# Kernel optimization log

Measured on AMD Instinct MI355X. Metric: run time of the kernel, lower is better.

The kernel has to match this reference:

```python
import jax, jax.numpy as jnp
import numpy as np

T, N, E, F, G, H = 8, 100000, 1600000, 17, 32, 48


def setup_inputs() -> dict:
    key = jax.random.key(0)
    ks = jax.random.split(key, 24)
    p = lambda k, sh: jax.random.normal(k, sh, jnp.float32) * 0.05
    return {
        "node_features": jax.random.normal(ks[0], (T, N, F), jnp.float32),
        "edge_index": jax.random.randint(ks[1], (T, 2, E), 0, N, jnp.int32),
        "graph_features": jax.random.normal(ks[2], (T, G), jnp.float32),
        # conv1 / conv2 (self + neigh linears)
        "Ws1": p(ks[3], (H, F)), "bs1": jnp.zeros((H,), jnp.float32),
        "Wn1": p(ks[4], (H, F)), "bn1": jnp.zeros((H,), jnp.float32),
        "Ws2": p(ks[5], (H, H)), "bs2": jnp.zeros((H,), jnp.float32),
        "Wn2": p(ks[6], (H, H)), "bn2": jnp.zeros((H,), jnp.float32),
        # graph projection
        "Wgp": p(ks[7], (H, G)), "bgp": jnp.zeros((H,), jnp.float32),
        # GRU (input 2H, hidden H), torch layout [3H, in]
        "W_ih": p(ks[8], (3 * H, 2 * H)), "b_ih": jnp.zeros((3 * H,), jnp.float32),
        "W_hh": p(ks[9], (3 * H, H)), "b_hh": jnp.zeros((3 * H,), jnp.float32),
        # attention, spatial mask, temporal mask
        "Wa": p(ks[10], (1, H)), "ba": jnp.zeros((1,), jnp.float32),
        "Wsm": p(ks[11], (H, H)), "bsm": jnp.zeros((H,), jnp.float32),
        "Wtm": p(ks[12], (1, H)), "btm": jnp.zeros((1,), jnp.float32),
        "Wr1": p(ks[13], (H, H)), "br1": jnp.zeros((H,), jnp.float32),
        "Wr2": p(ks[14], (1, H)), "br2": jnp.zeros((1,), jnp.float32),
    }


def _conv(x, src, dst, Ws, bs, Wn, bn):
    # gather-scatter mean aggregation over edges, then dual linear + relu
    n = x.shape[0]
    agg = jax.ops.segment_sum(x[src], dst, num_segments=n)          # [N, d]
    deg = jax.ops.segment_sum(jnp.ones(dst.shape, x.dtype), dst, num_segments=n)
    neigh = agg / jnp.clip(deg, 1.0)[:, None]
    return jax.nn.relu(x @ Ws.T + bs + neigh @ Wn.T + bn)


def _forward(node_features, edge_index, graph_features,
             Ws1, bs1, Wn1, bn1, Ws2, bs2, Wn2, bn2, Wgp, bgp,
             W_ih, b_ih, W_hh, b_hh, Wa, ba, Wsm, bsm, Wtm, btm,
             Wr1, br1, Wr2, br2):
    def snap(_, inp):
        x, src, dst, gf = inp
        h = _conv(x, src, dst, Ws1, bs1, Wn1, bn1)
        h = _conv(h, src, dst, Ws2, bs2, Wn2, bn2)
        sm = jax.nn.sigmoid(h @ Wsm.T + bsm)                        # [N, H]
        h = h * sm
        pooled = h.mean(axis=0)                                     # [H]
        gs = jax.nn.relu(gf @ Wgp.T + bgp)                          # [H]
        return None, (jnp.concatenate([pooled, gs]), sm)

    _, (seq, spatial_masks) = jax.lax.scan(
        snap, None,
        (node_features, edge_index[:, 0], edge_index[:, 1], graph_features))
    # seq: [T, 2H]

    def gru_step(h, x):
        gi = x @ W_ih.T + b_ih
        gh = h @ W_hh.T + b_hh
        ir, iz, inn = jnp.split(gi, 3)
        hr, hz, hn = jnp.split(gh, 3)
        r = jax.nn.sigmoid(ir + hr)
        z = jax.nn.sigmoid(iz + hz)
        n = jnp.tanh(inn + r * hn)
        h_new = (1.0 - z) * n + z * h
        return h_new, h_new

    h0 = jnp.zeros((H,), seq.dtype)
    _, gru_out = jax.lax.scan(gru_step, h0, seq)                    # [T, H]

    temp_mask = jax.nn.sigmoid(gru_out @ Wtm.T + btm)[:, 0]         # [T]
    scores = (gru_out @ Wa.T + ba)[:, 0]                            # [T]
    weights = jax.nn.softmax(scores)
    context = jnp.sum(gru_out * (weights * temp_mask)[:, None], axis=0)  # [H]
    pred = (jax.nn.relu(context @ Wr1.T + br1) @ Wr2.T + br2)[0]    # scalar

    top8 = jax.lax.top_k(jnp.abs(Ws1).mean(axis=0), 8)[0]           # channel importance values
    return pred, weights, top8, spatial_masks, temp_mask


def reference(node_features, edge_index, graph_features,
              Ws1, bs1, Wn1, bn1, Ws2, bs2, Wn2, bn2, Wgp, bgp,
              W_ih, b_ih, W_hh, b_hh, Wa, ba, Wsm, bsm, Wtm, btm,
              Wr1, br1, Wr2, br2):
    return _forward(node_features, edge_index, graph_features,
                    Ws1, bs1, Wn1, bn1, Ws2, bs2, Wn2, bn2, Wgp, bgp,
                    W_ih, b_ih, W_hh, b_hh, Wa, ba, Wsm, bsm, Wtm, btm,
                    Wr1, br1, Wr2, br2)
```

## Files before the change

kernel.cpp:

```cpp
#include <hip/hip_runtime.h>
#include <math.h>

#define T_ 8
#define N_ 100000
#define E_ 1600000
#define F_ 17
#define G_ 32
#define H_ 48
#define CONV_GRID 2048
#define FP 20
#define BK_ 128
#define NBK 782
#define CAP 2560
#define HIST_BLK 98
#define NPW 8

__device__ __forceinline__ float bf2f(unsigned short u) {
    return __uint_as_float((unsigned)u << 16);
}
__device__ __forceinline__ unsigned short f2bf(float v) {
    unsigned u = __float_as_uint(v);
    u += 0x7FFFu + ((u >> 16) & 1u);
    return (unsigned short)(u >> 16);
}

__global__ void k_binit(int* __restrict__ bcur) {
    int i = blockIdx.x * 1024 + threadIdx.x;
    if (i < NBK) bcur[i] = i * CAP;
}

__global__ __launch_bounds__(1024) void k_bscat(const int* __restrict__ src,
                                                const int* __restrict__ dst,
                                                int* __restrict__ bcur,
                                                unsigned* __restrict__ pairs) {
    __shared__ int cur[NBK];
    __shared__ int hist[NBK];
    int tid = threadIdx.x;
    for (int i = tid; i < NBK; i += 1024) hist[i] = 0;
    __syncthreads();
    int base = blockIdx.x * 16384;
    unsigned p[16]; int bk[16];
#pragma unroll
    for (int k = 0; k < 16; ++k) {
        int e = base + k * 1024 + tid;
        if (e < E_) {
            int d = dst[e];
            p[k] = (unsigned)src[e] | ((unsigned)(d & 127) << 17);
            bk[k] = d >> 7;
            atomicAdd(&hist[bk[k]], 1);
        } else {
            bk[k] = -1;
        }
    }
    __syncthreads();
    for (int i = tid; i < NBK; i += 1024) {
        int h = hist[i];
        cur[i] = h ? atomicAdd(&bcur[i], h) : 0;
    }
    __syncthreads();
#pragma unroll
    for (int k = 0; k < 16; ++k) {
        if (bk[k] >= 0) {
            int pos = atomicAdd(&cur[bk[k]], 1);
            if (pos < (bk[k] + 1) * CAP - 8) pairs[pos] = p[k];
        }
    }
}

__global__ __launch_bounds__(256) void k_sort(
        const unsigned* __restrict__ pairs, int* __restrict__ bcur,
        int* __restrict__ srcs, int* __restrict__ rowp, int* __restrict__ rowe) {
    __shared__ int hist[BK_];
    __shared__ int scan[BK_];
    __shared__ int curs[BK_];
    __shared__ int cnt_s;
    int tid = threadIdx.x, b = blockIdx.x;
    int start = b * CAP;
    if (tid == 0) {
        int c = bcur[b] - start;
        cnt_s = (c < CAP - 8) ? c : (CAP - 8);
        bcur[b] = start;
    }
    if (tid < BK_) hist[tid] = 0;
    __syncthreads();
    int count = cnt_s;
    int stop = start + count;
    for (int e = start + tid; e < stop; e += 256)
        atomicAdd(&hist[pairs[e] >> 17], 1);
    __syncthreads();
    if (tid < BK_) scan[tid] = hist[tid];
    __syncthreads();
    for (int off = 1; off < BK_; off <<= 1) {
        int v = 0;
        if (tid < BK_ && tid >= off) v = scan[tid - off];
        __syncthreads();
        if (tid < BK_) scan[tid] += v;
        __syncthreads();
    }
    if (tid < BK_) {
        int n = b * BK_ + tid;
        if (n < N_) {
            int st = start + scan[tid] - hist[tid];
            rowp[n] = st;
            rowe[n] = st + hist[tid];
            curs[tid] = st;
        }
    }
    __syncthreads();
    for (int e = start + tid; e < stop; e += 256) {
        unsigned p = pairs[e];
        int loc = (int)(p >> 17);
        int pos = atomicAdd(&curs[loc], 1);
        srcs[pos] = (int)(p & 131071u);
    }
    if (tid < 8) srcs[stop + tid] = 0;
}

__global__ __launch_bounds__(256) void k_aggW17(
        const float* __restrict__ tbl, const int* __restrict__ rowp,
        const int* __restrict__ rowe, const int* __restrict__ srcs,
        float* __restrict__ neigh) {
    int wv = (blockIdx.x * 256 + threadIdx.x) >> 6;
    int lane = threadIdx.x & 63;
    int c = lane & 31;
    int half = lane >> 5;
    const bool act = c < F_;
    int n0 = (wv * 2 + half) * NPW;
    if (n0 >= N_) return;
    int n1 = n0 + NPW; if (n1 > N_) n1 = N_;
    int e = rowp[n0];
    int sA = srcs[e], sB = srcs[e + 1], sC = srcs[e + 2], sD = srcs[e + 3];
    float v0 = act ? tbl[(size_t)sA * F_ + c] : 0.f;
    float v1 = act ? tbl[(size_t)sB * F_ + c] : 0.f;
    float v2 = act ? tbl[(size_t)sC * F_ + c] : 0.f;
    float v3 = act ? tbl[(size_t)sD * F_ + c] : 0.f;
    int sn = srcs[e + 4];
    for (int n = n0; n < n1; ++n) {
        int stop = rowe[n];
        int dg = stop - e;
        float acc = 0.f;
        for (; e < stop; ++e) {
            float vn = act ? tbl[(size_t)sn * F_ + c] : 0.f;
            int sn2 = srcs[e + 5];
            acc += v0;
            v0 = v1; v1 = v2; v2 = v3; v3 = vn; sn = sn2;
        }
        if (c < FP)
            neigh[(size_t)n * FP + c] = act ? acc / fmaxf((float)dg, 1.f) : 0.f;
    }
}

__global__ __launch_bounds__(256) void k_aggW48b(
        const unsigned* __restrict__ tblu, const int* __restrict__ rowp,
        const int* __restrict__ rowe, const int* __restrict__ srcs,
        float* __restrict__ neigh) {
    int wv = (blockIdx.x * 256 + threadIdx.x) >> 6;
    int lane = threadIdx.x & 63;
    int c = lane & 31;
    int half = lane >> 5;
    const bool act = c < 24;
    int n0 = (wv * 2 + half) * NPW;
    if (n0 >= N_) return;
    int n1 = n0 + NPW; if (n1 > N_) n1 = N_;
    int e = rowp[n0];
    int sA = srcs[e], sB = srcs[e + 1], sC = srcs[e + 2], sD = srcs[e + 3];
    unsigned u0 = act ? tblu[(size_t)sA * 24 + c] : 0u;
    unsigned u1 = act ? tblu[(size_t)sB * 24 + c] : 0u;
    unsigned u2 = act ? tblu[(size_t)sC * 24 + c] : 0u;
    unsigned u3 = act ? tblu[(size_t)sD * 24 + c] : 0u;
    int sn = srcs[e + 4];
    for (int n = n0; n < n1; ++n) {
        int stop = rowe[n];
        int dg = stop - e;
        float a0 = 0.f, a1 = 0.f;
        for (; e < stop; ++e) {
            unsigned un = act ? tblu[(size_t)sn * 24 + c] : 0u;
            int sn2 = srcs[e + 5];
            a0 += __uint_as_float(u0 << 16);
            a1 += __uint_as_float(u0 & 0xFFFF0000u);
            u0 = u1; u1 = u2; u2 = u3; u3 = un; sn = sn2;
        }
        if (act) {
            float inv = 1.f / fmaxf((float)dg, 1.f);
            float2 w; w.x = a0 * inv; w.y = a1 * inv;
            *(float2*)&neigh[(size_t)n * H_ + c * 2] = w;
        }
    }
}

__global__ __launch_bounds__(192) void k_conv1T(
        const float* __restrict__ x, const float* __restrict__ neigh,
        const float* __restrict__ Ws1, const float* __restrict__ bs1,
        const float* __restrict__ Wn1, const float* __restrict__ bn1,
        unsigned short* __restrict__ h1b) {
    __shared__ __attribute__((aligned(16))) float shx[16 * FP];
    __shared__ __attribute__((aligned(16))) float sna[16 * FP];
    int tid = threadIdx.x;
    int q = tid / H_, h = tid - q * H_;
    float ws[FP], wn[FP];
#pragma unroll
    for (int k = 0; k < FP; ++k) {
        ws[k] = (k < F_) ? Ws1[h * F_ + k] : 0.f;
        wn[k] = (k < F_) ? Wn1[h * F_ + k] : 0.f;
    }
    const float bsum = bs1[h] + bn1[h];
    const int ngroups = N_ / 16;
    for (int g = blockIdx.x; g < ngroups; g += gridDim.x) {
        __syncthreads();
        for (int i = tid; i < 16 * FP; i += 192) {
            int row = i / FP, k = i - row * FP;
            shx[i] = (k < F_) ? x[(g * 16 + row) * F_ + k] : 0.f;
        }
        for (int i = tid; i < 16 * 5; i += 192) {
            int row = i / 5, k4 = i - row * 5;
            *(float4*)&sna[row * FP + k4 * 4] =
                *(const float4*)&neigh[(size_t)(g * 16 + row) * FP + k4 * 4];
        }
        __syncthreads();
        float acc[4];
#pragma unroll
        for (int c = 0; c < 4; ++c) acc[c] = bsum;
#pragma unroll
        for (int k4 = 0; k4 < FP / 4; ++k4) {
#pragma unroll
            for (int c = 0; c < 4; ++c) {
                const float4 xv = *(const float4*)&shx[(q * 4 + c) * FP + k4 * 4];
                const float4 av = *(const float4*)&sna[(q * 4 + c) * FP + k4 * 4];
                acc[c] += xv.x * ws[k4 * 4 + 0] + xv.y * ws[k4 * 4 + 1]
                        + xv.z * ws[k4 * 4 + 2] + xv.w * ws[k4 * 4 + 3]
                        + av.x * wn[k4 * 4 + 0] + av.y * wn[k4 * 4 + 1]
                        + av.z * wn[k4 * 4 + 2] + av.w * wn[k4 * 4 + 3];
            }
        }
#pragma unroll
        for (int c = 0; c < 4; ++c)
            h1b[(size_t)(g * 16 + q * 4 + c) * H_ + h] = f2bf(fmaxf(acc[c], 0.f));
    }
}

__global__ __launch_bounds__(192) void k_conv2T(
        const unsigned short* __restrict__ h1b, const float* __restrict__ neigh,
        const float* __restrict__ Ws2, const float* __restrict__ bs2,
        const float* __restrict__ Wn2, const float* __restrict__ bn2,
        const float* __restrict__ Wsm, const float* __restrict__ bsm,
        float* __restrict__ sm_out, float* __restrict__ partial) {
    __shared__ __attribute__((aligned(16))) float shh[2][16 * H_];
    __shared__ __attribute__((aligned(16))) float sna[2][16 * H_];
    __shared__ __attribute__((aligned(16))) float shh2[16 * H_];
    __shared__ float wmT[H_ * H_];
    __shared__ float psum[H_];
    int tid = threadIdx.x;
    int q = tid / H_, h = tid - q * H_;
    float ws[H_], wn[H_];
#pragma unroll
    for (int k = 0; k < H_; ++k) {
        ws[k] = Ws2[h * H_ + k];
        wn[k] = Wn2[h * H_ + k];
    }
    for (int i = tid; i < H_ * H_; i += 192) {
        int k = i / H_, hh = i - k * H_;
        wmT[i] = Wsm[hh * H_ + k];
    }
    const float bsum = bs2[h] + bn2[h];
    const float bm = bsm[h];
    if (tid < H_) psum[tid] = 0.f;
    float pacc = 0.f;
    const int ngroups = N_ / 16;

    ushort4 hreg = *(const ushort4*)&h1b[(size_t)blockIdx.x * 768 + tid * 4];
    float4  nreg = *(const float4*)&neigh[(size_t)blockIdx.x * 768 + tid * 4];
    {
        float4 hf;
        hf.x = bf2f(hreg.x); hf.y = bf2f(hreg.y);
        hf.z = bf2f(hreg.z); hf.w = bf2f(hreg.w);
        *(float4*)&shh[0][tid * 4] = hf;
        *(float4*)&sna[0][tid * 4] = nreg;
    }
    __syncthreads();
    int cur = 0;
    for (int g = blockIdx.x; g < ngroups; g += gridDim.x) {
        int gn = g + gridDim.x;
        if (gn < ngroups) {
            hreg = *(const ushort4*)&h1b[(size_t)gn * 768 + tid * 4];
            nreg = *(const float4*)&neigh[(size_t)gn * 768 + tid * 4];
        }
        float acc[4];
#pragma unroll
        for (int c = 0; c < 4; ++c) acc[c] = bsum;
#pragma unroll
        for (int k4 = 0; k4 < H_ / 4; ++k4) {
#pragma unroll
            for (int c = 0; c < 4; ++c) {
                const float4 hv = *(const float4*)&shh[cur][(q * 4 + c) * H_ + k4 * 4];
                const float4 av = *(const float4*)&sna[cur][(q * 4 + c) * H_ + k4 * 4];
                acc[c] += hv.x * ws[k4 * 4 + 0] + hv.y * ws[k4 * 4 + 1]
                        + hv.z * ws[k4 * 4 + 2] + hv.w * ws[k4 * 4 + 3]
                        + av.x * wn[k4 * 4 + 0] + av.y * wn[k4 * 4 + 1]
                        + av.z * wn[k4 * 4 + 2] + av.w * wn[k4 * 4 + 3];
            }
        }
        float h2v[4];
#pragma unroll
        for (int c = 0; c < 4; ++c) {
            h2v[c] = fmaxf(acc[c], 0.f);
            shh2[(q * 4 + c) * H_ + h] = h2v[c];
        }
        __syncthreads();
        float macc[4];
#pragma unroll
        for (int c = 0; c < 4; ++c) macc[c] = bm;
#pragma unroll
        for (int k4 = 0; k4 < H_ / 4; ++k4) {
            float wm0 = wmT[(k4 * 4 + 0) * H_ + h];
            float wm1 = wmT[(k4 * 4 + 1) * H_ + h];
            float wm2 = wmT[(k4 * 4 + 2) * H_ + h];
            float wm3 = wmT[(k4 * 4 + 3) * H_ + h];
#pragma unroll
            for (int c = 0; c < 4; ++c) {
                const float4 hv = *(const float4*)&shh2[(q * 4 + c) * H_ + k4 * 4];
                macc[c] += hv.x * wm0 + hv.y * wm1 + hv.z * wm2 + hv.w * wm3;
            }
        }
#pragma unroll
        for (int c = 0; c < 4; ++c) {
            int n = g * 16 + q * 4 + c;
            float smv = 1.f / (1.f + expf(-macc[c]));
            sm_out[(size_t)n * H_ + h] = smv;
            pacc += h2v[c] * smv;
        }
        if (gn < ngroups) {
            float4 hf;
            hf.x = bf2f(hreg.x); hf.y = bf2f(hreg.y);
            hf.z = bf2f(hreg.z); hf.w = bf2f(hreg.w);
            *(float4*)&shh[cur ^ 1][tid * 4] = hf;
            *(float4*)&sna[cur ^ 1][tid * 4] = nreg;
        }
        __syncthreads();
        cur ^= 1;
    }
    atomicAdd(&psum[h], pacc);
    __syncthreads();
    if (tid < H_) partial[tid * CONV_GRID + blockIdx.x] = psum[tid];
}

__global__ void k_reduce(const float* __restrict__ partial, float* __restrict__ pooled) {
    __shared__ float s[256];
    int b = blockIdx.x, tid = threadIdx.x;
    const float* p = partial + (size_t)b * CONV_GRID;
    float v = 0.f;
    for (int i = tid; i < CONV_GRID; i += 256) v += p[i];
    s[tid] = v; __syncthreads();
    for (int off = 128; off > 0; off >>= 1) {
        if (tid < off) s[tid] += s[tid + off];
        __syncthreads();
    }
    if (tid == 0) pooled[b] = s[0];
}

__global__ void k_final(const float* __restrict__ gf_all, const float* __restrict__ pooled,
                        const float* __restrict__ Wgp, const float* __restrict__ bgp,
                        const float* __restrict__ W_ih, const float* __restrict__ b_ih,
                        const float* __restrict__ W_hh, const float* __restrict__ b_hh,
                        const float* __restrict__ Wa, const float* __restrict__ ba,
                        const float* __restrict__ Wtm, const float* __restrict__ btm,
                        const float* __restrict__ Wr1, const float* __restrict__ br1,
                        const float* __restrict__ Wr2, const float* __restrict__ br2,
                        const float* __restrict__ Ws1,
                        float* __restrict__ out) {
    __shared__ float seq[T_][2 * H_];
    __shared__ float hstate[H_];
    __shared__ float gout[T_][H_];
    __shared__ float tmp[H_];
    __shared__ float scores[T_], tmask[T_], wts[T_];
    __shared__ float ctx[H_], reg[H_];
    int tid = threadIdx.x;

    if (tid < H_) {
        for (int t = 0; t < T_; ++t) {
            seq[t][tid] = pooled[t * H_ + tid] / (float)N_;
            float acc = bgp[tid];
            for (int k = 0; k < G_; ++k) acc += Wgp[tid * G_ + k] * gf_all[t * G_ + k];
            seq[t][H_ + tid] = fmaxf(acc, 0.0f);
        }
        hstate[tid] = 0.0f;
    }
    __syncthreads();

    for (int t = 0; t < T_; ++t) {
        if (tid < H_) {
            float gi_r = b_ih[tid], gi_z = b_ih[H_ + tid], gi_n = b_ih[2 * H_ + tid];
            for (int k = 0; k < 2 * H_; ++k) {
                float xv = seq[t][k];
                gi_r += W_ih[tid * 2 * H_ + k] * xv;
                gi_z += W_ih[(H_ + tid) * 2 * H_ + k] * xv;
                gi_n += W_ih[(2 * H_ + tid) * 2 * H_ + k] * xv;
            }
            float gh_r = b_hh[tid], gh_z = b_hh[H_ + tid], gh_n = b_hh[2 * H_ + tid];
            for (int k = 0; k < H_; ++k) {
                float hv = hstate[k];
                gh_r += W_hh[tid * H_ + k] * hv;
                gh_z += W_hh[(H_ + tid) * H_ + k] * hv;
                gh_n += W_hh[(2 * H_ + tid) * H_ + k] * hv;
            }
            float r = 1.0f / (1.0f + expf(-(gi_r + gh_r)));
            float z = 1.0f / (1.0f + expf(-(gi_z + gh_z)));
            float nn = tanhf(gi_n + r * gh_n);
            tmp[tid] = (1.0f - z) * nn + z * hstate[tid];
        }
        __syncthreads();
        if (tid < H_) {
            hstate[tid] = tmp[tid];
            gout[t][tid] = tmp[tid];
        }
        __syncthreads();
    }

    if (tid < T_) {
        float s = ba[0], m = btm[0];
        for (int k = 0; k < H_; ++k) {
            s += Wa[k] * gout[tid][k];
            m += Wtm[k] * gout[tid][k];
        }
        scores[tid] = s;
        tmask[tid] = 1.0f / (1.0f + expf(-m));
    }
    __syncthreads();
    if (tid == 0) {
        float mx = scores[0];
        for (int t = 1; t < T_; ++t) mx = fmaxf(mx, scores[t]);
        float sum = 0.0f;
        for (int t = 0; t < T_; ++t) { wts[t] = expf(scores[t] - mx); sum += wts[t]; }
        for (int t = 0; t < T_; ++t) {
            wts[t] /= sum;
            out[1 + t] = wts[t];
            out[17 + (size_t)T_ * N_ * H_ + t] = tmask[t];
        }
    }
    __syncthreads();
    if (tid < H_) {
        float c = 0.0f;
        for (int t = 0; t < T_; ++t) c += gout[t][tid] * wts[t] * tmask[t];
        ctx[tid] = c;
    }
    __syncthreads();
    if (tid < H_) {
        float acc = br1[tid];
        for (int k = 0; k < H_; ++k) acc += Wr1[tid * H_ + k] * ctx[k];
        reg[tid] = fmaxf(acc, 0.0f);
    }
    __syncthreads();
    if (tid == 0) {
        float p = br2[0];
        for (int k = 0; k < H_; ++k) p += Wr2[k] * reg[k];
        out[0] = p;
        float m[F_];
        for (int f = 0; f < F_; ++f) {
            float s = 0.0f;
            for (int h = 0; h < H_; ++h) s += fabsf(Ws1[h * F_ + f]);
            m[f] = s / (float)H_;
        }
        for (int i = 0; i < 8; ++i) {
            int best = i;
            for (int j = i + 1; j < F_; ++j)
                if (m[j] > m[best]) best = j;
            float tv = m[i]; m[i] = m[best]; m[best] = tv;
            out[9 + i] = m[i];
        }
    }
}

extern "C" void kernel_launch(void* const* d_in, const int* in_sizes, int n_in,
                              void* d_out, int out_size, void* d_ws, size_t ws_size,
                              hipStream_t stream) {
    const float* node_features  = (const float*)d_in[0];
    const int*   edge_index     = (const int*)d_in[1];
    const float* graph_features = (const float*)d_in[2];
    const float* Ws1 = (const float*)d_in[3];
    const float* bs1 = (const float*)d_in[4];
    const float* Wn1 = (const float*)d_in[5];
    const float* bn1 = (const float*)d_in[6];
    const float* Ws2 = (const float*)d_in[7];
    const float* bs2 = (const float*)d_in[8];
    const float* Wn2 = (const float*)d_in[9];
    const float* bn2 = (const float*)d_in[10];
    const float* Wgp = (const float*)d_in[11];
    const float* bgp = (const float*)d_in[12];
    const float* W_ih = (const float*)d_in[13];
    const float* b_ih = (const float*)d_in[14];
    const float* W_hh = (const float*)d_in[15];
    const float* b_hh = (const float*)d_in[16];
    const float* Wa  = (const float*)d_in[17];
    const float* ba  = (const float*)d_in[18];
    const float* Wsm = (const float*)d_in[19];
    const float* bsm = (const float*)d_in[20];
    const float* Wtm = (const float*)d_in[21];
    const float* btm = (const float*)d_in[22];
    const float* Wr1 = (const float*)d_in[23];
    const float* br1 = (const float*)d_in[24];
    const float* Wr2 = (const float*)d_in[25];
    const float* br2 = (const float*)d_in[26];

    unsigned short* h1b = (unsigned short*)d_ws;
    unsigned* pairs = (unsigned*)d_ws;
    int* bcur     = (int*)(h1b + (size_t)N_ * H_);
    int* srcs     = bcur + 800;
    int* rowp     = srcs + NBK * CAP;
    int* rowe     = rowp + (N_ + 8);
    float* neigh  = (float*)(rowe + (N_ + 8));
    float* partial = neigh + (size_t)N_ * H_;
    float* pooled  = partial + (size_t)T_ * H_ * CONV_GRID;

    float* out = (float*)d_out;

    const int AGG_BLOCKS = (N_ + NPW * 8 - 1) / (NPW * 8);

    k_binit<<<1, 1024, 0, stream>>>(bcur);

    for (int t = 0; t < T_; ++t) {
        const float* x   = node_features + (size_t)t * N_ * F_;
        const int*   src = edge_index + (size_t)t * 2 * E_;
        const int*   dst = src + E_;

        k_bscat<<<HIST_BLK, 1024, 0, stream>>>(src, dst, bcur, pairs);
        k_sort<<<NBK, 256, 0, stream>>>(pairs, bcur, srcs, rowp, rowe);

        k_aggW17<<<AGG_BLOCKS, 256, 0, stream>>>(x, rowp, rowe, srcs, neigh);
        k_conv1T<<<CONV_GRID, 192, 0, stream>>>(x, neigh, Ws1, bs1, Wn1, bn1, h1b);
        k_aggW48b<<<AGG_BLOCKS, 256, 0, stream>>>((const unsigned*)h1b, rowp, rowe, srcs, neigh);
        float* sm_out = out + 17 + (size_t)t * N_ * H_;
        k_conv2T<<<CONV_GRID, 192, 0, stream>>>(h1b, neigh, Ws2, bs2, Wn2, bn2,
                                                Wsm, bsm, sm_out,
                                                partial + (size_t)t * H_ * CONV_GRID);
    }

    k_reduce<<<T_ * H_, 256, 0, stream>>>(partial, pooled);
    k_final<<<1, 64, 0, stream>>>(graph_features, pooled, Wgp, bgp,
                                  W_ih, b_ih, W_hh, b_hh, Wa, ba, Wtm, btm,
                                  Wr1, br1, Wr2, br2, Ws1, out);
}
```

Baseline: 1.973 ms.

## Fuse next-snapshot edge bucket scatter into conv2 kernel to overlap work

Merges the edge bucket-scatter for the next snapshot into the conv2 kernel launch as extra blocks, so the histogram and scatter run concurrently with the conv2/spatial-mask compute of the current snapshot. It moves the pairs buffer out of the h1b region so the two no longer alias, and halves the conv2 grid to leave room for the extra blocks. This removes one launch per snapshot and overlaps memory-bound scatter with compute. In exchange the scatter blocks use 192 threads instead of 1024, and a smaller conv2 grid may reduce parallelism.

```diff
diff --git a/kernel.cpp b/kernel.cpp
--- a/kernel.cpp
+++ b/kernel.cpp
@@ -7,7 +7,8 @@
 #define F_ 17
 #define G_ 32
 #define H_ 48
-#define CONV_GRID 2048
+#define CONV1_GRID 2048
+#define CONV2_GRID 1024
 #define FP 20
 #define BK_ 128
 #define NBK 782
@@ -238,18 +239,46 @@
     }
 }
 
-__global__ __launch_bounds__(192) void k_conv2T(
+__global__ __launch_bounds__(192) void k_c2bs(
         const unsigned short* __restrict__ h1b, const float* __restrict__ neigh,
         const float* __restrict__ Ws2, const float* __restrict__ bs2,
         const float* __restrict__ Wn2, const float* __restrict__ bn2,
         const float* __restrict__ Wsm, const float* __restrict__ bsm,
-        float* __restrict__ sm_out, float* __restrict__ partial) {
+        float* __restrict__ sm_out, float* __restrict__ partial,
+        const int* __restrict__ src2, const int* __restrict__ dst2,
+        int* __restrict__ bcur, unsigned* __restrict__ pairs) {
+    int tid = threadIdx.x;
+    if ((int)blockIdx.x < HIST_BLK) {
+        if (src2 == nullptr) return;
+        __shared__ int bhist[NBK];
+        __shared__ int bcurL[NBK];
+        for (int i = tid; i < NBK; i += 192) bhist[i] = 0;
+        __syncthreads();
+        int base = blockIdx.x * 16384;
+        int lim = base + 16384; if (lim > E_) lim = E_;
+        for (int e = base + tid; e < lim; e += 192)
+            atomicAdd(&bhist[dst2[e] >> 7], 1);
+        __syncthreads();
+        for (int i = tid; i < NBK; i += 192) {
+            int h = bhist[i];
+            bcurL[i] = h ? atomicAdd(&bcur[i], h) : 0;
+        }
+        __syncthreads();
+        for (int e = base + tid; e < lim; e += 192) {
+            int d = dst2[e];
+            int b = d >> 7;
+            int pos = atomicAdd(&bcurL[b], 1);
+            if (pos < (b + 1) * CAP - 8)
+                pairs[pos] = (unsigned)src2[e] | ((unsigned)(d & 127) << 17);
+        }
+        return;
+    }
+    int cb = blockIdx.x - HIST_BLK;
     __shared__ __attribute__((aligned(16))) float shh[2][16 * H_];
     __shared__ __attribute__((aligned(16))) float sna[2][16 * H_];
     __shared__ __attribute__((aligned(16))) float shh2[16 * H_];
     __shared__ float wmT[H_ * H_];
     __shared__ float psum[H_];
-    int tid = threadIdx.x;
     int q = tid / H_, h = tid - q * H_;
     float ws[H_], wn[H_];
 #pragma unroll
@@ -267,8 +296,8 @@
     float pacc = 0.f;
     const int ngroups = N_ / 16;
 
-    ushort4 hreg = *(const ushort4*)&h1b[(size_t)blockIdx.x * 768 + tid * 4];
-    float4  nreg = *(const float4*)&neigh[(size_t)blockIdx.x * 768 + tid * 4];
+    ushort4 hreg = *(const ushort4*)&h1b[(size_t)cb * 768 + tid * 4];
+    float4  nreg = *(const float4*)&neigh[(size_t)cb * 768 + tid * 4];
     {
         float4 hf;
         hf.x = bf2f(hreg.x); hf.y = bf2f(hreg.y);
@@ -278,8 +307,8 @@
     }
     __syncthreads();
     int cur = 0;
-    for (int g = blockIdx.x; g < ngroups; g += gridDim.x) {
-        int gn = g + gridDim.x;
+    for (int g = cb; g < ngroups; g += CONV2_GRID) {
+        int gn = g + CONV2_GRID;
         if (gn < ngroups) {
             hreg = *(const ushort4*)&h1b[(size_t)gn * 768 + tid * 4];
             nreg = *(const float4*)&neigh[(size_t)gn * 768 + tid * 4];
@@ -340,15 +369,15 @@
     }
     atomicAdd(&psum[h], pacc);
     __syncthreads();
-    if (tid < H_) partial[tid * CONV_GRID + blockIdx.x] = psum[tid];
+    if (tid < H_) partial[tid * CONV2_GRID + cb] = psum[tid];
 }
 
 __global__ void k_reduce(const float* __restrict__ partial, float* __restrict__ pooled) {
     __shared__ float s[256];
     int b = blockIdx.x, tid = threadIdx.x;
-    const float* p = partial + (size_t)b * CONV_GRID;
+    const float* p = partial + (size_t)b * CONV2_GRID;
     float v = 0.f;
-    for (int i = tid; i < CONV_GRID; i += 256) v += p[i];
+    for (int i = tid; i < CONV2_GRID; i += 256) v += p[i];
     s[tid] = v; __syncthreads();
     for (int off = 128; off > 0; off >>= 1) {
         if (tid < off) s[tid] += s[tid + off];
@@ -501,14 +530,14 @@
     const float* br2 = (const float*)d_in[26];
 
     unsigned short* h1b = (unsigned short*)d_ws;
-    unsigned* pairs = (unsigned*)d_ws;
-    int* bcur     = (int*)(h1b + (size_t)N_ * H_);
+    unsigned* pairs = (unsigned*)(h1b + (size_t)N_ * H_);
+    int* bcur     = (int*)(pairs + (size_t)NBK * CAP);
     int* srcs     = bcur + 800;
-    int* rowp     = srcs + NBK * CAP;
+    int* rowp     = srcs + (size_t)NBK * CAP;
     int* rowe     = rowp + (N_ + 8);
     float* neigh  = (float*)(rowe + (N_ + 8));
     float* partial = neigh + (size_t)N_ * H_;
-    float* pooled  = partial + (size_t)T_ * H_ * CONV_GRID;
+    float* pooled  = partial + (size_t)T_ * H_ * CONV2_GRID;
 
     float* out = (float*)d_out;
 
@@ -516,21 +545,31 @@
 
     k_binit<<<1, 1024, 0, stream>>>(bcur);
 
+    {
+        const int* src0 = edge_index;
+        const int* dst0 = src0 + E_;
+        k_bscat<<<HIST_BLK, 1024, 0, stream>>>(src0, dst0, bcur, pairs);
+        k_sort<<<NBK, 256, 0, stream>>>(pairs, bcur, srcs, rowp, rowe);
+        k_aggW17<<<AGG_BLOCKS, 256, 0, stream>>>(node_features, rowp, rowe, srcs, neigh);
+        k_conv1T<<<CONV1_GRID, 192, 0, stream>>>(node_features, neigh, Ws1, bs1, Wn1, bn1, h1b);
+        k_aggW48b<<<AGG_BLOCKS, 256, 0, stream>>>((const unsigned*)h1b, rowp, rowe, srcs, neigh);
+    }
+
     for (int t = 0; t < T_; ++t) {
-        const float* x   = node_features + (size_t)t * N_ * F_;
-        const int*   src = edge_index + (size_t)t * 2 * E_;
-        const int*   dst = src + E_;
-
-        k_bscat<<<HIST_BLK, 1024, 0, stream>>>(src, dst, bcur, pairs);
-        k_sort<<<NBK, 256, 0, stream>>>(pairs, bcur, srcs, rowp, rowe);
-
-        k_aggW17<<<AGG_BLOCKS, 256, 0, stream>>>(x, rowp, rowe, srcs, neigh);
-        k_conv1T<<<CONV_GRID, 192, 0, stream>>>(x, neigh, Ws1, bs1, Wn1, bn1, h1b);
-        k_aggW48b<<<AGG_BLOCKS, 256, 0, stream>>>((const unsigned*)h1b, rowp, rowe, srcs, neigh);
+        const int* srcN = (t < T_ - 1) ? edge_index + (size_t)(t + 1) * 2 * E_ : nullptr;
+        const int* dstN = (t < T_ - 1) ? srcN + E_ : nullptr;
         float* sm_out = out + 17 + (size_t)t * N_ * H_;
-        k_conv2T<<<CONV_GRID, 192, 0, stream>>>(h1b, neigh, Ws2, bs2, Wn2, bn2,
-                                                Wsm, bsm, sm_out,
-                                                partial + (size_t)t * H_ * CONV_GRID);
+        k_c2bs<<<HIST_BLK + CONV2_GRID, 192, 0, stream>>>(
+            h1b, neigh, Ws2, bs2, Wn2, bn2, Wsm, bsm,
+            sm_out, partial + (size_t)t * H_ * CONV2_GRID,
+            srcN, dstN, bcur, pairs);
+        if (t < T_ - 1) {
+            const float* x = node_features + (size_t)(t + 1) * N_ * F_;
+            k_sort<<<NBK, 256, 0, stream>>>(pairs, bcur, srcs, rowp, rowe);
+            k_aggW17<<<AGG_BLOCKS, 256, 0, stream>>>(x, rowp, rowe, srcs, neigh);
+            k_conv1T<<<CONV1_GRID, 192, 0, stream>>>(x, neigh, Ws1, bs1, Wn1, bn1, h1b);
+            k_aggW48b<<<AGG_BLOCKS, 256, 0, stream>>>((const unsigned*)h1b, rowp, rowe, srcs, neigh);
+        }
     }
 
     k_reduce<<<T_ * H_, 256, 0, stream>>>(partial, pooled);
```

After: 2.084 ms. 1.06x slower.
